# Performance work log

Hardware: AMD Instinct MI355X
Metric: run time of the kernel (lower is better)

Reference implementation:

```python
import jax, jax.numpy as jnp
import numpy as np

N = 50000        # nodes
DEG = 16         # fixed out-degree per row (CSR)
E = N * DEG      # edges
H = 4            # attention heads
D = 32           # head feature dim
NEG_SLOPE = 0.2  # GAT leaky-relu slope (scalar hyperparam from forward args)


def setup_inputs() -> dict:
    key = jax.random.key(0)
    k1, k2, k3, k4 = jax.random.split(key, 4)
    attn_row = jax.random.normal(k1, (N, H), dtype=jnp.float32)   # a_dst . Wh_i per head
    attn_col = jax.random.normal(k2, (N, H), dtype=jnp.float32)   # a_src . Wh_j per head
    in_feat = jax.random.normal(k3, (N, H, D), dtype=jnp.float32)  # transformed node feats
    col_indices = jax.random.randint(k4, (E,), 0, N, dtype=jnp.int32)
    row_indptr = (jnp.arange(N + 1, dtype=jnp.int32) * DEG)        # CSR pointers, fixed degree
    return {
        "attn_row": attn_row,
        "attn_col": attn_col,
        "in_feat": in_feat,
        "row_indptr": row_indptr,
        "col_indices": col_indices,
    }


def reference(attn_row, attn_col, in_feat, row_indptr, col_indices):
    # Fused GAT: per-edge score = leaky_relu(attn_row[i] + attn_col[j]),
    # softmax over each destination row's edges, then weighted sparse aggregation.
    n = attn_row.shape[0]
    e = col_indices.shape[0]
    # row id of each edge from CSR indptr (jit-safe, static edge count)
    row_ids = jnp.searchsorted(row_indptr, jnp.arange(e, dtype=row_indptr.dtype), side="right") - 1
    score = jax.nn.leaky_relu(attn_row[row_ids] + attn_col[col_indices], NEG_SLOPE)  # [E,H]
    # numerically-stable edge softmax per destination row
    m = jax.ops.segment_max(score, row_ids, num_segments=n)        # [N,H]
    ex = jnp.exp(score - m[row_ids])                               # [E,H]
    denom = jax.ops.segment_sum(ex, row_ids, num_segments=n)       # [N,H]
    alpha = ex / denom[row_ids]                                    # [E,H]
    # gather neighbor features, weight, scatter-add to destinations
    msg = alpha[:, :, None] * in_feat[col_indices]                 # [E,H,D]
    out = jax.ops.segment_sum(msg, row_ids, num_segments=n)        # [N,H,D]
    return out
```

## Files before the change

### kernel.cpp

```cpp
#include <hip/hip_runtime.h>
#include <math.h>


#define GAT_H 4
#define GAT_D 32
#define GAT_DEG 16
#define GAT_NEG_SLOPE 0.2f

__global__ __launch_bounds__(256, 4) void gat_fused_kernel(
    const float* __restrict__ attn_row,
    const float* __restrict__ attn_col,
    const float* __restrict__ in_feat,
    const int*   __restrict__ row_indptr,
    const int*   __restrict__ col_indices,
    float*       __restrict__ out,
    int n)
{
    const int wave_id = (int)((blockIdx.x * (unsigned)blockDim.x + threadIdx.x) >> 6);
    const int lane    = threadIdx.x & 63;
    if (wave_id >= n) return;
    const int i = wave_id;

    const int start = row_indptr[i];
    const int deg   = row_indptr[i + 1] - start;

    const int e = lane & 15;
    const int h = lane >> 4;

    float s    = -INFINITY;
    int   colv = 0;
    if (e < deg) {
        colv = col_indices[start + e];
        const float ar = attn_row[i * GAT_H + h];
        const float ac = attn_col[colv * GAT_H + h];
        const float x  = ar + ac;
        s = (x > 0.0f) ? x : GAT_NEG_SLOPE * x;
    }

    float m = s;
    #pragma unroll
    for (int off = 1; off < 16; off <<= 1)
        m = fmaxf(m, __shfl_xor(m, off));

    const float ex = (e < deg) ? __expf(s - m) : 0.0f;

    float denom = ex;
    #pragma unroll
    for (int off = 1; off < 16; off <<= 1)
        denom += __shfl_xor(denom, off);

    const float alpha = ex * __builtin_amdgcn_rcpf(denom);

    const int d0   = (lane & 15) * 2;
    const int base = lane & 48;

    float2 f[GAT_DEG];
    float  a[GAT_DEG];
    #pragma unroll
    for (int k = 0; k < GAT_DEG; ++k) {
        const int idx = __shfl(colv, base + k);
        a[k] = __shfl(alpha, base + k);
        f[k] = *reinterpret_cast<const float2*>(
            &in_feat[(long)idx * (GAT_H * GAT_D) + h * GAT_D + d0]);
    }

    float accx = 0.0f, accy = 0.0f;
    #pragma unroll
    for (int k = 0; k < GAT_DEG; ++k) {
        accx = fmaf(a[k], f[k].x, accx);
        accy = fmaf(a[k], f[k].y, accy);
    }

    *reinterpret_cast<float2*>(&out[(long)i * (GAT_H * GAT_D) + h * GAT_D + d0]) =
        make_float2(accx, accy);
}

extern "C" void kernel_launch(void* const* d_in, const int* in_sizes, int n_in,
                              void* d_out, int out_size, void* d_ws, size_t ws_size,
                              hipStream_t stream) {
    const float* attn_row    = (const float*)d_in[0];
    const float* attn_col    = (const float*)d_in[1];
    const float* in_feat     = (const float*)d_in[2];
    const int*   row_indptr  = (const int*)d_in[3];
    const int*   col_indices = (const int*)d_in[4];
    float*       out         = (float*)d_out;

    const int n = in_sizes[0] / GAT_H;

    const int threads = 256;
    const int nodes_per_block = threads / 64;
    const int blocks = (n + nodes_per_block - 1) / nodes_per_block;

    gat_fused_kernel<<<blocks, threads, 0, stream>>>(
        attn_row, attn_col, in_feat, row_indptr, col_indices, out, n);
}
```

Measured before the change: 136.8 us.

## Load column indices per lane and issue feature gathers before softmax

Each lane now loads all 16 column indices with vectorized int4 loads and computes the per-edge softmax redundantly in registers, removing the cross-lane shuffles. The feature gathers are issued right after the index loads, so they no longer wait on the attention-score loads and reductions. Normalization by the denominator is moved to a single multiply at the output. In exchange the kernel uses more registers and issues redundant scalar loads of attn_col. It also assumes every row has exactly 16 edges and 16-byte-aligned row starts, since it always reads 16 indices.

```diff
diff --git a/kernel.cpp b/kernel.cpp
--- a/kernel.cpp
+++ b/kernel.cpp
@@ -19,50 +19,56 @@
     const int wave_id = (int)((blockIdx.x * (unsigned)blockDim.x + threadIdx.x) >> 6);
     const int lane    = threadIdx.x & 63;
     if (wave_id >= n) return;
-    const int i = wave_id;
+    const int i  = wave_id;
+    const int h  = lane >> 4;
+    const int d0 = (lane & 15) * 2;
 
-    const int start = row_indptr[i];
-    const int deg   = row_indptr[i + 1] - start;
+    int start = row_indptr[i];
+    const int deg = row_indptr[i + 1] - start;
+    start = __builtin_amdgcn_readfirstlane(start);
 
-    const int e = lane & 15;
-    const int h = lane >> 4;
-
-    float s    = -INFINITY;
-    int   colv = 0;
-    if (e < deg) {
-        colv = col_indices[start + e];
-        const float ar = attn_row[i * GAT_H + h];
-        const float ac = attn_col[colv * GAT_H + h];
-        const float x  = ar + ac;
-        s = (x > 0.0f) ? x : GAT_NEG_SLOPE * x;
+    int idx[GAT_DEG];
+    {
+        const int4* cip = reinterpret_cast<const int4*>(col_indices + start);
+        #pragma unroll
+        for (int q = 0; q < 4; ++q) {
+            const int4 c = cip[q];
+            idx[4 * q + 0] = c.x;
+            idx[4 * q + 1] = c.y;
+            idx[4 * q + 2] = c.z;
+            idx[4 * q + 3] = c.w;
+        }
     }
 
-    float m = s;
-    #pragma unroll
-    for (int off = 1; off < 16; off <<= 1)
-        m = fmaxf(m, __shfl_xor(m, off));
-
-    const float ex = (e < deg) ? __expf(s - m) : 0.0f;
-
-    float denom = ex;
-    #pragma unroll
-    for (int off = 1; off < 16; off <<= 1)
-        denom += __shfl_xor(denom, off);
-
-    const float alpha = ex * __builtin_amdgcn_rcpf(denom);
-
-    const int d0   = (lane & 15) * 2;
-    const int base = lane & 48;
-
     float2 f[GAT_DEG];
-    float  a[GAT_DEG];
     #pragma unroll
     for (int k = 0; k < GAT_DEG; ++k) {
-        const int idx = __shfl(colv, base + k);
-        a[k] = __shfl(alpha, base + k);
         f[k] = *reinterpret_cast<const float2*>(
-            &in_feat[(long)idx * (GAT_H * GAT_D) + h * GAT_D + d0]);
+            &in_feat[(long)idx[k] * (GAT_H * GAT_D) + h * GAT_D + d0]);
     }
+
+    const float ar = attn_row[i * GAT_H + h];
+    float s[GAT_DEG];
+    #pragma unroll
+    for (int k = 0; k < GAT_DEG; ++k) {
+        const float ac = attn_col[idx[k] * GAT_H + h];
+        const float x  = ar + ac;
+        const float lr = (x > 0.0f) ? x : GAT_NEG_SLOPE * x;
+        s[k] = (k < deg) ? lr : -INFINITY;
+    }
+
+    float m = s[0];
+    #pragma unroll
+    for (int k = 1; k < GAT_DEG; ++k) m = fmaxf(m, s[k]);
+
+    float a[GAT_DEG];
+    float denom = 0.0f;
+    #pragma unroll
+    for (int k = 0; k < GAT_DEG; ++k) {
+        a[k] = __expf(s[k] - m);
+        denom += a[k];
+    }
+    const float rdenom = __builtin_amdgcn_rcpf(denom);
 
     float accx = 0.0f, accy = 0.0f;
     #pragma unroll
@@ -72,7 +78,7 @@
     }
 
     *reinterpret_cast<float2*>(&out[(long)i * (GAT_H * GAT_D) + h * GAT_D + d0]) =
-        make_float2(accx, accy);
+        make_float2(accx * rdenom, accy * rdenom);
 }
 
 extern "C" void kernel_launch(void* const* d_in, const int* in_sizes, int n_in,
```

Result: no change. 135.6 us (-0.9%).
